# Performance work log

Measured on AMD Instinct MI355X. Metric: run time of the kernel, lower is better.

The kernel has to match this reference:

```python
import jax, jax.numpy as jnp
import numpy as np

H = 4096  # hidden_size == input_size


def setup_inputs() -> dict:
    key = jax.random.key(0)
    ks = jax.random.split(key, 12)
    s = 0.02  # weight init scale
    return {
        "x": jax.random.normal(ks[0], (H,), jnp.float32),
        "h_prev": jnp.zeros((H,), jnp.float32),
        "C_prev": jax.random.normal(ks[1], (H, H), jnp.float32) * 0.01,
        "n_prev": jax.random.uniform(ks[2], (H,), jnp.float32) + 1.0,
        # projection weights (hidden_size x input_size) and biases
        "Wq": jax.random.normal(ks[3], (H, H), jnp.float32) * s,
        "Wk": jax.random.normal(ks[4], (H, H), jnp.float32) * s,
        "Wv": jax.random.normal(ks[5], (H, H), jnp.float32) * s,
        "Wo": jax.random.normal(ks[6], (H, H), jnp.float32) * s,
        "bq": jnp.zeros((H,), jnp.float32),
        "bk": jnp.zeros((H,), jnp.float32),
        "bv": jnp.zeros((H,), jnp.float32),
        "bo": jnp.zeros((H,), jnp.float32),
        # scalar input/forget gates: w^T x + b
        "wi": jax.random.normal(ks[7], (H,), jnp.float32) * s,
        "bi": jnp.zeros((), jnp.float32),
        "wf": jax.random.normal(ks[8], (H,), jnp.float32) * s,
        "bf": jnp.ones((), jnp.float32),  # bias forget gate toward remembering
    }


def reference(x, h_prev, C_prev, n_prev, Wq, Wk, Wv, Wo,
              bq, bk, bv, bo, wi, bi, wf, bf):
    # mLSTM single-step cell (xLSTM matrix memory). h_prev is unused by the
    # mLSTM math (no hidden-to-hidden recurrence), matching the CUDA layer API.
    d = jnp.asarray(Wk.shape[0], x.dtype)
    q = Wq @ x + bq                                   # [H]
    k = (Wk @ x + bk) / jnp.sqrt(d)                   # [H], scaled key
    v = Wv @ x + bv                                   # [H]
    i_gate = jnp.exp(jnp.dot(wi, x) + bi)             # scalar exponential input gate
    f_gate = jax.nn.sigmoid(jnp.dot(wf, x) + bf)      # scalar sigmoid forget gate
    # covariance-style rank-1 matrix-memory update
    C = f_gate * C_prev + i_gate * jnp.outer(v, k)    # [H, H]
    n = f_gate * n_prev + i_gate * k                  # [H]
    # normalized readout
    denom = jnp.maximum(jnp.abs(jnp.dot(n, q)), jnp.asarray(1.0, x.dtype))
    h_tilde = (C @ q) / denom                         # [H]
    o_gate = jax.nn.sigmoid(Wo @ x + bo)              # [H] output gate
    h = o_gate * h_tilde
    return (h, C, n)
```

## Files before the change

kernel.cpp:

```cpp
#include <hip/hip_runtime.h>
#include <math.h>

#define H 4096
#define HWORDS4 (H / 4)
#define ITERS (HWORDS4 / 64)

__device__ __forceinline__ float wave_reduce_sum(float v) {
    #pragma unroll
    for (int off = 32; off > 0; off >>= 1)
        v += __shfl_down(v, off, 64);
    return v;
}

__device__ __forceinline__ float sigmoidf_(float x) {
    return 1.0f / (1.0f + __expf(-x));
}

__global__ __launch_bounds__(256) void gemv_all(
    const float* __restrict__ x,
    const float* __restrict__ Wq, const float* __restrict__ Wk,
    const float* __restrict__ Wv, const float* __restrict__ Wo,
    const float* __restrict__ bq, const float* __restrict__ bk,
    const float* __restrict__ bv, const float* __restrict__ bo,
    const float* __restrict__ wi, const float* __restrict__ wf,
    float* __restrict__ q, float* __restrict__ k,
    float* __restrict__ v, float* __restrict__ og,
    float* __restrict__ s2)
{
    const int wave = threadIdx.x >> 6;
    const int lane = threadIdx.x & 63;
    const int rowId = blockIdx.x * 4 + wave;
    if (rowId >= 4 * H + 2) return;

    const int m = rowId >> 12;
    const int r = rowId & (H - 1);

    const float* row;
    if (rowId < 4 * H) {
        const float* W = (m == 0) ? Wq : (m == 1) ? Wk : (m == 2) ? Wv : Wo;
        row = W + (size_t)r * H;
    } else {
        row = (rowId == 4 * H) ? wi : wf;
    }

    const float4* row4 = (const float4*)row;
    const float4* x4   = (const float4*)x;

    float sum = 0.0f;
    #pragma unroll
    for (int it = 0; it < ITERS; ++it) {
        const int idx = it * 64 + lane;
        float4 a = row4[idx];
        float4 b = x4[idx];
        sum += a.x * b.x + a.y * b.y + a.z * b.z + a.w * b.w;
    }
    sum = wave_reduce_sum(sum);

    if (lane == 0) {
        if (rowId < 4 * H) {
            if (m == 0)      q[r]  = sum + bq[r];
            else if (m == 1) k[r]  = (sum + bk[r]) * 0.015625f;
            else if (m == 2) v[r]  = sum + bv[r];
            else             og[r] = sigmoidf_(sum + bo[r]);
        } else {
            s2[rowId - 4 * H] = sum;
        }
    }
}

__global__ __launch_bounds__(256) void c_update(
    const float* __restrict__ C_prev,
    const float* __restrict__ q, const float* __restrict__ k,
    const float* __restrict__ v, const float* __restrict__ s2,
    const float* __restrict__ bi, const float* __restrict__ bf,
    float* __restrict__ C_out, float* __restrict__ u)
{
    const int wave = threadIdx.x >> 6;
    const int lane = threadIdx.x & 63;
    const int r = blockIdx.x * 4 + wave;

    const float ig = __expf(s2[0] + bi[0]);
    const float fg = sigmoidf_(s2[1] + bf[0]);
    const float ivr = ig * v[r];

    const float4* c4 = (const float4*)(C_prev + (size_t)r * H);
    float4*       o4 = (float4*)(C_out + (size_t)r * H);
    const float4* q4 = (const float4*)q;
    const float4* k4 = (const float4*)k;

    float acc = 0.0f;
    #pragma unroll
    for (int it = 0; it < ITERS; ++it) {
        const int idx = it * 64 + lane;
        float4 c  = c4[idx];
        float4 qq = q4[idx];
        float4 kk = k4[idx];
        float4 o;
        o.x = fg * c.x + ivr * kk.x;
        o.y = fg * c.y + ivr * kk.y;
        o.z = fg * c.z + ivr * kk.z;
        o.w = fg * c.w + ivr * kk.w;
        o4[idx] = o;
        acc += c.x * qq.x + c.y * qq.y + c.z * qq.z + c.w * qq.w;
    }
    acc = wave_reduce_sum(acc);
    if (lane == 0) u[r] = acc;
}

__global__ __launch_bounds__(1024) void finalize(
    const float* __restrict__ n_prev,
    const float* __restrict__ q, const float* __restrict__ k,
    const float* __restrict__ v, const float* __restrict__ og,
    const float* __restrict__ u, const float* __restrict__ s2,
    const float* __restrict__ bi, const float* __restrict__ bf,
    float* __restrict__ h, float* __restrict__ n_out)
{
    const int t = threadIdx.x;
    const int wave = t >> 6;
    const int lane = t & 63;

    const float ig = __expf(s2[0] + bi[0]);
    const float fg = sigmoidf_(s2[1] + bf[0]);

    float nq = 0.0f, kq = 0.0f;
    for (int j = t; j < H; j += 1024) {
        float kj = k[j];
        float qj = q[j];
        float nj = fg * n_prev[j] + ig * kj;
        n_out[j] = nj;
        nq += nj * qj;
        kq += kj * qj;
    }
    nq = wave_reduce_sum(nq);
    kq = wave_reduce_sum(kq);

    __shared__ float snq[16], skq[16];
    if (lane == 0) { snq[wave] = nq; skq[wave] = kq; }
    __syncthreads();
    if (t == 0) {
        float a = 0.0f, b = 0.0f;
        #pragma unroll
        for (int w = 0; w < 16; ++w) { a += snq[w]; b += skq[w]; }
        snq[0] = a; skq[0] = b;
    }
    __syncthreads();

    const float denom = fmaxf(fabsf(snq[0]), 1.0f);
    const float kqv = skq[0];
    const float inv_denom = 1.0f / denom;

    for (int j = t; j < H; j += 1024) {
        float ht = (fg * u[j] + ig * v[j] * kqv) * inv_denom;
        h[j] = og[j] * ht;
    }
}

extern "C" void kernel_launch(void* const* d_in, const int* in_sizes, int n_in,
                              void* d_out, int out_size, void* d_ws, size_t ws_size,
                              hipStream_t stream) {
    const float* x      = (const float*)d_in[0];
    const float* C_prev = (const float*)d_in[2];
    const float* n_prev = (const float*)d_in[3];
    const float* Wq     = (const float*)d_in[4];
    const float* Wk     = (const float*)d_in[5];
    const float* Wv     = (const float*)d_in[6];
    const float* Wo     = (const float*)d_in[7];
    const float* bq     = (const float*)d_in[8];
    const float* bk     = (const float*)d_in[9];
    const float* bv     = (const float*)d_in[10];
    const float* bo     = (const float*)d_in[11];
    const float* wi     = (const float*)d_in[12];
    const float* bi     = (const float*)d_in[13];
    const float* wf     = (const float*)d_in[14];
    const float* bf     = (const float*)d_in[15];

    float* out   = (float*)d_out;
    float* h_out = out;
    float* C_out = out + H;
    float* n_out = out + H + (size_t)H * H;

    float* ws = (float*)d_ws;
    float* q  = ws;
    float* k  = ws + H;
    float* v  = ws + 2 * H;
    float* og = ws + 3 * H;
    float* u  = ws + 4 * H;
    float* s2 = ws + 5 * H;

    const int nrows = 4 * H + 2;
    const int blocks1 = (nrows + 3) / 4;
    gemv_all<<<blocks1, 256, 0, stream>>>(x, Wq, Wk, Wv, Wo, bq, bk, bv, bo,
                                          wi, wf, q, k, v, og, s2);

    c_update<<<H / 4, 256, 0, stream>>>(C_prev, q, k, v, s2, bi, bf, C_out, u);

    finalize<<<1, 1024, 0, stream>>>(n_prev, q, k, v, og, u, s2, bi, bf,
                                     h_out, n_out);
}
```

Baseline: 339.7 us.

## Use whole-block rows with register-cached x/q/k vectors in GEMV and C update

Both memory-bound kernels now assign full 256-thread blocks to process two rows at a time, eight rows per block. The shared vectors (x, or q and k) are loaded into registers once per block instead of being re-read per row by each wave. Cross-wave results are combined through shared memory and barriers. This cuts redundant vector loads and gives each thread more independent loads in flight. The cost is two __syncthreads per row pair, higher register pressure, and half as many blocks.

```diff
diff --git a/kernel.cpp b/kernel.cpp
--- a/kernel.cpp
+++ b/kernel.cpp
@@ -2,8 +2,10 @@
 #include <math.h>
 
 #define H 4096
-#define HWORDS4 (H / 4)
-#define ITERS (HWORDS4 / 64)
+#define H4 (H / 4)
+#define T1 256
+#define RPB 8
+#define NB1 (4 * H / RPB)
 
 __device__ __forceinline__ float wave_reduce_sum(float v) {
     #pragma unroll
@@ -16,7 +18,11 @@
     return 1.0f / (1.0f + __expf(-x));
 }
 
-__global__ __launch_bounds__(256) void gemv_all(
+__device__ __forceinline__ float dot4(float4 a, float4 b) {
+    return a.x * b.x + a.y * b.y + a.z * b.z + a.w * b.w;
+}
+
+__global__ __launch_bounds__(T1) void gemv_all(
     const float* __restrict__ x,
     const float* __restrict__ Wq, const float* __restrict__ Wk,
     const float* __restrict__ Wv, const float* __restrict__ Wo,
@@ -27,84 +33,144 @@
     float* __restrict__ v, float* __restrict__ og,
     float* __restrict__ s2)
 {
-    const int wave = threadIdx.x >> 6;
-    const int lane = threadIdx.x & 63;
-    const int rowId = blockIdx.x * 4 + wave;
-    if (rowId >= 4 * H + 2) return;
-
-    const int m = rowId >> 12;
-    const int r = rowId & (H - 1);
-
-    const float* row;
-    if (rowId < 4 * H) {
-        const float* W = (m == 0) ? Wq : (m == 1) ? Wk : (m == 2) ? Wv : Wo;
-        row = W + (size_t)r * H;
-    } else {
-        row = (rowId == 4 * H) ? wi : wf;
-    }
-
-    const float4* row4 = (const float4*)row;
-    const float4* x4   = (const float4*)x;
-
-    float sum = 0.0f;
+    const int tid  = threadIdx.x;
+    const int wave = tid >> 6;
+    const int lane = tid & 63;
+
+    __shared__ float red[2][4];
+
+    const float4* x4 = (const float4*)x;
+    float4 xr0 = x4[tid];
+    float4 xr1 = x4[tid + 256];
+    float4 xr2 = x4[tid + 512];
+    float4 xr3 = x4[tid + 768];
+
+    if (blockIdx.x == NB1) {
+        const float4* a4 = (const float4*)wi;
+        const float4* b4 = (const float4*)wf;
+        float4 a0 = a4[tid], a1 = a4[tid + 256], a2 = a4[tid + 512], a3 = a4[tid + 768];
+        float4 c0 = b4[tid], c1 = b4[tid + 256], c2 = b4[tid + 512], c3 = b4[tid + 768];
+        float sa = dot4(a0, xr0) + dot4(a1, xr1) + dot4(a2, xr2) + dot4(a3, xr3);
+        float sb = dot4(c0, xr0) + dot4(c1, xr1) + dot4(c2, xr2) + dot4(c3, xr3);
+        sa = wave_reduce_sum(sa);
+        sb = wave_reduce_sum(sb);
+        if (lane == 0) { red[0][wave] = sa; red[1][wave] = sb; }
+        __syncthreads();
+        if (tid < 2) {
+            float s = red[tid][0] + red[tid][1] + red[tid][2] + red[tid][3];
+            s2[tid] = s;
+        }
+        return;
+    }
+
+    const int row0 = blockIdx.x * RPB;
+    const int m = row0 >> 12;
+    const float* W    = (m == 0) ? Wq : (m == 1) ? Wk : (m == 2) ? Wv : Wo;
+    const float* bias = (m == 0) ? bq : (m == 1) ? bk : (m == 2) ? bv : bo;
+    const int rbase = row0 & (H - 1);
+
     #pragma unroll
-    for (int it = 0; it < ITERS; ++it) {
-        const int idx = it * 64 + lane;
-        float4 a = row4[idx];
-        float4 b = x4[idx];
-        sum += a.x * b.x + a.y * b.y + a.z * b.z + a.w * b.w;
-    }
-    sum = wave_reduce_sum(sum);
-
-    if (lane == 0) {
-        if (rowId < 4 * H) {
-            if (m == 0)      q[r]  = sum + bq[r];
-            else if (m == 1) k[r]  = (sum + bk[r]) * 0.015625f;
-            else if (m == 2) v[r]  = sum + bv[r];
-            else             og[r] = sigmoidf_(sum + bo[r]);
-        } else {
-            s2[rowId - 4 * H] = sum;
+    for (int rr = 0; rr < RPB; rr += 2) {
+        const float4* a4 = (const float4*)(W + (size_t)(rbase + rr) * H);
+        const float4* b4 = (const float4*)(W + (size_t)(rbase + rr + 1) * H);
+        float4 a0 = a4[tid], a1 = a4[tid + 256], a2 = a4[tid + 512], a3 = a4[tid + 768];
+        float4 c0 = b4[tid], c1 = b4[tid + 256], c2 = b4[tid + 512], c3 = b4[tid + 768];
+
+        float sa = dot4(a0, xr0) + dot4(a1, xr1) + dot4(a2, xr2) + dot4(a3, xr3);
+        float sb = dot4(c0, xr0) + dot4(c1, xr1) + dot4(c2, xr2) + dot4(c3, xr3);
+        sa = wave_reduce_sum(sa);
+        sb = wave_reduce_sum(sb);
+        if (lane == 0) { red[0][wave] = sa; red[1][wave] = sb; }
+        __syncthreads();
+        if (tid < 2) {
+            const float s = red[tid][0] + red[tid][1] + red[tid][2] + red[tid][3];
+            const int r = rbase + rr + tid;
+            const float sbias = s + bias[r];
+            if (m == 0)      q[r]  = sbias;
+            else if (m == 1) k[r]  = sbias * 0.015625f;
+            else if (m == 2) v[r]  = sbias;
+            else             og[r] = sigmoidf_(sbias);
         }
-    }
-}
-
-__global__ __launch_bounds__(256) void c_update(
+        __syncthreads();
+    }
+}
+
+__global__ __launch_bounds__(T1) void c_update(
     const float* __restrict__ C_prev,
     const float* __restrict__ q, const float* __restrict__ k,
     const float* __restrict__ v, const float* __restrict__ s2,
     const float* __restrict__ bi, const float* __restrict__ bf,
     float* __restrict__ C_out, float* __restrict__ u)
 {
-    const int wave = threadIdx.x >> 6;
-    const int lane = threadIdx.x & 63;
-    const int r = blockIdx.x * 4 + wave;
+    const int tid  = threadIdx.x;
+    const int wave = tid >> 6;
+    const int lane = tid & 63;
+
+    __shared__ float red[2][4];
 
     const float ig = __expf(s2[0] + bi[0]);
     const float fg = sigmoidf_(s2[1] + bf[0]);
-    const float ivr = ig * v[r];
-
-    const float4* c4 = (const float4*)(C_prev + (size_t)r * H);
-    float4*       o4 = (float4*)(C_out + (size_t)r * H);
+
     const float4* q4 = (const float4*)q;
     const float4* k4 = (const float4*)k;
-
-    float acc = 0.0f;
+    float4 qr0 = q4[tid], qr1 = q4[tid + 256], qr2 = q4[tid + 512], qr3 = q4[tid + 768];
+    float4 kr0 = k4[tid], kr1 = k4[tid + 256], kr2 = k4[tid + 512], kr3 = k4[tid + 768];
+
+    const int row0 = blockIdx.x * RPB;
+
     #pragma unroll
-    for (int it = 0; it < ITERS; ++it) {
-        const int idx = it * 64 + lane;
-        float4 c  = c4[idx];
-        float4 qq = q4[idx];
-        float4 kk = k4[idx];
+    for (int rr = 0; rr < RPB; rr += 2) {
+        const int ra = row0 + rr;
+        const int rb = ra + 1;
+        const float iva = ig * v[ra];
+        const float ivb = ig * v[rb];
+
+        const float4* ca4 = (const float4*)(C_prev + (size_t)ra * H);
+        const float4* cb4 = (const float4*)(C_prev + (size_t)rb * H);
+        float4*       oa4 = (float4*)(C_out + (size_t)ra * H);
+        float4*       ob4 = (float4*)(C_out + (size_t)rb * H);
+
+        float4 a0 = ca4[tid], a1 = ca4[tid + 256], a2 = ca4[tid + 512], a3 = ca4[tid + 768];
+        float4 c0 = cb4[tid], c1 = cb4[tid + 256], c2 = cb4[tid + 512], c3 = cb4[tid + 768];
+
         float4 o;
-        o.x = fg * c.x + ivr * kk.x;
-        o.y = fg * c.y + ivr * kk.y;
-        o.z = fg * c.z + ivr * kk.z;
-        o.w = fg * c.w + ivr * kk.w;
-        o4[idx] = o;
-        acc += c.x * qq.x + c.y * qq.y + c.z * qq.z + c.w * qq.w;
-    }
-    acc = wave_reduce_sum(acc);
-    if (lane == 0) u[r] = acc;
+        o.x = fg * a0.x + iva * kr0.x; o.y = fg * a0.y + iva * kr0.y;
+        o.z = fg * a0.z + iva * kr0.z; o.w = fg * a0.w + iva * kr0.w;
+        oa4[tid] = o;
+        o.x = fg * a1.x + iva * kr1.x; o.y = fg * a1.y + iva * kr1.y;
+        o.z = fg * a1.z + iva * kr1.z; o.w = fg * a1.w + iva * kr1.w;
+        oa4[tid + 256] = o;
+        o.x = fg * a2.x + iva * kr2.x; o.y = fg * a2.y + iva * kr2.y;
+        o.z = fg * a2.z + iva * kr2.z; o.w = fg * a2.w + iva * kr2.w;
+        oa4[tid + 512] = o;
+        o.x = fg * a3.x + iva * kr3.x; o.y = fg * a3.y + iva * kr3.y;
+        o.z = fg * a3.z + iva * kr3.z; o.w = fg * a3.w + iva * kr3.w;
+        oa4[tid + 768] = o;
+
+        o.x = fg * c0.x + ivb * kr0.x; o.y = fg * c0.y + ivb * kr0.y;
+        o.z = fg * c0.z + ivb * kr0.z; o.w = fg * c0.w + ivb * kr0.w;
+        ob4[tid] = o;
+        o.x = fg * c1.x + ivb * kr1.x; o.y = fg * c1.y + ivb * kr1.y;
+        o.z = fg * c1.z + ivb * kr1.z; o.w = fg * c1.w + ivb * kr1.w;
+        ob4[tid + 256] = o;
+        o.x = fg * c2.x + ivb * kr2.x; o.y = fg * c2.y + ivb * kr2.y;
+        o.z = fg * c2.z + ivb * kr2.z; o.w = fg * c2.w + ivb * kr2.w;
+        ob4[tid + 512] = o;
+        o.x = fg * c3.x + ivb * kr3.x; o.y = fg * c3.y + ivb * kr3.y;
+        o.z = fg * c3.z + ivb * kr3.z; o.w = fg * c3.w + ivb * kr3.w;
+        ob4[tid + 768] = o;
+
+        float sa = dot4(a0, qr0) + dot4(a1, qr1) + dot4(a2, qr2) + dot4(a3, qr3);
+        float sb = dot4(c0, qr0) + dot4(c1, qr1) + dot4(c2, qr2) + dot4(c3, qr3);
+        sa = wave_reduce_sum(sa);
+        sb = wave_reduce_sum(sb);
+        if (lane == 0) { red[0][wave] = sa; red[1][wave] = sb; }
+        __syncthreads();
+        if (tid < 2) {
+            u[row0 + rr + tid] = red[tid][0] + red[tid][1] + red[tid][2] + red[tid][3];
+        }
+        __syncthreads();
+    }
 }
 
 __global__ __launch_bounds__(1024) void finalize(
@@ -187,12 +253,10 @@
     float* u  = ws + 4 * H;
     float* s2 = ws + 5 * H;
 
-    const int nrows = 4 * H + 2;
-    const int blocks1 = (nrows + 3) / 4;
-    gemv_all<<<blocks1, 256, 0, stream>>>(x, Wq, Wk, Wv, Wo, bq, bk, bv, bo,
-                                          wi, wf, q, k, v, og, s2);
-
-    c_update<<<H / 4, 256, 0, stream>>>(C_prev, q, k, v, s2, bi, bf, C_out, u);
+    gemv_all<<<NB1 + 1, T1, 0, stream>>>(x, Wq, Wk, Wv, Wo, bq, bk, bv, bo,
+                                         wi, wf, q, k, v, og, s2);
+
+    c_update<<<H / RPB, T1, 0, stream>>>(C_prev, q, k, v, s2, bi, bf, C_out, u);
 
     finalize<<<1, 1024, 0, stream>>>(n_prev, q, k, v, og, u, s2, bi, bf,
                                      h_out, n_out);
```

Measured after the change: 348.0 us. 2.4% more time.

## Stage vectors in LDS, batch row loads, use nontemporal C accesses

Applied to the files above, without the earlier changes.

The GEMV and C-update kernels now copy x (and q, k) into shared memory once per block, and every global load of a row is issued up front in two groups separated by scheduling barriers, so many loads are in flight at once. The C_prev reads and C_out writes use nontemporal hints to avoid polluting the cache with streamed data. This aims to raise memory-level parallelism on the bandwidth-bound streams. The cost is 16 KB to 32 KB of LDS per block, which may limit occupancy, plus higher register pressure from 16 live float4 values.

```diff
diff --git a/kernel.cpp b/kernel.cpp
--- a/kernel.cpp
+++ b/kernel.cpp
@@ -2,8 +2,9 @@
 #include <math.h>
 
 #define H 4096
-#define HWORDS4 (H / 4)
-#define ITERS (HWORDS4 / 64)
+#define H4 (H / 4)
+
+typedef float f4 __attribute__((ext_vector_type(4)));
 
 __device__ __forceinline__ float wave_reduce_sum(float v) {
     #pragma unroll
@@ -14,6 +15,10 @@
 
 __device__ __forceinline__ float sigmoidf_(float x) {
     return 1.0f / (1.0f + __expf(-x));
+}
+
+__device__ __forceinline__ float dot4(f4 a, f4 b) {
+    return a.x * b.x + a.y * b.y + a.z * b.z + a.w * b.w;
 }
 
 __global__ __launch_bounds__(256) void gemv_all(
@@ -27,8 +32,16 @@
     float* __restrict__ v, float* __restrict__ og,
     float* __restrict__ s2)
 {
-    const int wave = threadIdx.x >> 6;
-    const int lane = threadIdx.x & 63;
+    const int tid  = threadIdx.x;
+    const int wave = tid >> 6;
+    const int lane = tid & 63;
+
+    __shared__ f4 xs[H4];
+    const f4* x4 = (const f4*)x;
+    #pragma unroll
+    for (int i = 0; i < 4; ++i) xs[tid + i * 256] = x4[tid + i * 256];
+    __syncthreads();
+
     const int rowId = blockIdx.x * 4 + wave;
     if (rowId >= 4 * H + 2) return;
 
@@ -42,28 +55,55 @@
     } else {
         row = (rowId == 4 * H) ? wi : wf;
     }
-
-    const float4* row4 = (const float4*)row;
-    const float4* x4   = (const float4*)x;
-
-    float sum = 0.0f;
-    #pragma unroll
-    for (int it = 0; it < ITERS; ++it) {
-        const int idx = it * 64 + lane;
-        float4 a = row4[idx];
-        float4 b = x4[idx];
-        sum += a.x * b.x + a.y * b.y + a.z * b.z + a.w * b.w;
-    }
-    sum = wave_reduce_sum(sum);
+    const f4* row4 = (const f4*)row;
+
+    f4 a0 = row4[lane +   0];
+    f4 a1 = row4[lane +  64];
+    f4 a2 = row4[lane + 128];
+    f4 a3 = row4[lane + 192];
+    f4 a4_ = row4[lane + 256];
+    f4 a5 = row4[lane + 320];
+    f4 a6 = row4[lane + 384];
+    f4 a7 = row4[lane + 448];
+    __builtin_amdgcn_sched_barrier(0);
+    f4 b0 = row4[lane + 512];
+    f4 b1 = row4[lane + 576];
+    f4 b2 = row4[lane + 640];
+    f4 b3 = row4[lane + 704];
+    f4 b4_ = row4[lane + 768];
+    f4 b5 = row4[lane + 832];
+    f4 b6 = row4[lane + 896];
+    f4 b7 = row4[lane + 960];
+    __builtin_amdgcn_sched_barrier(0);
+
+    float s = 0.0f;
+    s += dot4(a0,  xs[lane +   0]);
+    s += dot4(a1,  xs[lane +  64]);
+    s += dot4(a2,  xs[lane + 128]);
+    s += dot4(a3,  xs[lane + 192]);
+    s += dot4(a4_, xs[lane + 256]);
+    s += dot4(a5,  xs[lane + 320]);
+    s += dot4(a6,  xs[lane + 384]);
+    s += dot4(a7,  xs[lane + 448]);
+    s += dot4(b0,  xs[lane + 512]);
+    s += dot4(b1,  xs[lane + 576]);
+    s += dot4(b2,  xs[lane + 640]);
+    s += dot4(b3,  xs[lane + 704]);
+    s += dot4(b4_, xs[lane + 768]);
+    s += dot4(b5,  xs[lane + 832]);
+    s += dot4(b6,  xs[lane + 896]);
+    s += dot4(b7,  xs[lane + 960]);
+
+    s = wave_reduce_sum(s);
 
     if (lane == 0) {
         if (rowId < 4 * H) {
-            if (m == 0)      q[r]  = sum + bq[r];
-            else if (m == 1) k[r]  = (sum + bk[r]) * 0.015625f;
-            else if (m == 2) v[r]  = sum + bv[r];
-            else             og[r] = sigmoidf_(sum + bo[r]);
+            if (m == 0)      q[r]  = s + bq[r];
+            else if (m == 1) k[r]  = (s + bk[r]) * 0.015625f;
+            else if (m == 2) v[r]  = s + bv[r];
+            else             og[r] = sigmoidf_(s + bo[r]);
         } else {
-            s2[rowId - 4 * H] = sum;
+            s2[rowId - 4 * H] = s;
         }
     }
 }
@@ -75,34 +115,67 @@
     const float* __restrict__ bi, const float* __restrict__ bf,
     float* __restrict__ C_out, float* __restrict__ u)
 {
-    const int wave = threadIdx.x >> 6;
-    const int lane = threadIdx.x & 63;
+    const int tid  = threadIdx.x;
+    const int wave = tid >> 6;
+    const int lane = tid & 63;
+
+    __shared__ f4 qs[H4];
+    __shared__ f4 ks[H4];
+    const f4* q4 = (const f4*)q;
+    const f4* k4 = (const f4*)k;
+    #pragma unroll
+    for (int i = 0; i < 4; ++i) {
+        qs[tid + i * 256] = q4[tid + i * 256];
+        ks[tid + i * 256] = k4[tid + i * 256];
+    }
+    __syncthreads();
+
     const int r = blockIdx.x * 4 + wave;
 
-    const float ig = __expf(s2[0] + bi[0]);
-    const float fg = sigmoidf_(s2[1] + bf[0]);
+    const float ig  = __expf(s2[0] + bi[0]);
+    const float fg  = sigmoidf_(s2[1] + bf[0]);
     const float ivr = ig * v[r];
 
-    const float4* c4 = (const float4*)(C_prev + (size_t)r * H);
-    float4*       o4 = (float4*)(C_out + (size_t)r * H);
-    const float4* q4 = (const float4*)q;
-    const float4* k4 = (const float4*)k;
+    const f4* c4 = (const f4*)(C_prev + (size_t)r * H);
+    f4*       o4 = (f4*)(C_out + (size_t)r * H);
+
+    f4 a0 = __builtin_nontemporal_load(&c4[lane +   0]);
+    f4 a1 = __builtin_nontemporal_load(&c4[lane +  64]);
+    f4 a2 = __builtin_nontemporal_load(&c4[lane + 128]);
+    f4 a3 = __builtin_nontemporal_load(&c4[lane + 192]);
+    f4 a4_ = __builtin_nontemporal_load(&c4[lane + 256]);
+    f4 a5 = __builtin_nontemporal_load(&c4[lane + 320]);
+    f4 a6 = __builtin_nontemporal_load(&c4[lane + 384]);
+    f4 a7 = __builtin_nontemporal_load(&c4[lane + 448]);
+    __builtin_amdgcn_sched_barrier(0);
+    f4 b0 = __builtin_nontemporal_load(&c4[lane + 512]);
+    f4 b1 = __builtin_nontemporal_load(&c4[lane + 576]);
+    f4 b2 = __builtin_nontemporal_load(&c4[lane + 640]);
+    f4 b3 = __builtin_nontemporal_load(&c4[lane + 704]);
+    f4 b4_ = __builtin_nontemporal_load(&c4[lane + 768]);
+    f4 b5 = __builtin_nontemporal_load(&c4[lane + 832]);
+    f4 b6 = __builtin_nontemporal_load(&c4[lane + 896]);
+    f4 b7 = __builtin_nontemporal_load(&c4[lane + 960]);
+    __builtin_amdgcn_sched_barrier(0);
 
     float acc = 0.0f;
-    #pragma unroll
-    for (int it = 0; it < ITERS; ++it) {
-        const int idx = it * 64 + lane;
-        float4 c  = c4[idx];
-        float4 qq = q4[idx];
-        float4 kk = k4[idx];
-        float4 o;
-        o.x = fg * c.x + ivr * kk.x;
-        o.y = fg * c.y + ivr * kk.y;
-        o.z = fg * c.z + ivr * kk.z;
-        o.w = fg * c.w + ivr * kk.w;
-        o4[idx] = o;
-        acc += c.x * qq.x + c.y * qq.y + c.z * qq.z + c.w * qq.w;
-    }
+    f4 o;
+    #define CONSUME(reg, off)                                            \
+        {                                                                \
+            f4 kk = ks[lane + (off)];                                    \
+            o.x = fg * reg.x + ivr * kk.x;                               \
+            o.y = fg * reg.y + ivr * kk.y;                               \
+            o.z = fg * reg.z + ivr * kk.z;                               \
+            o.w = fg * reg.w + ivr * kk.w;                               \
+            __builtin_nontemporal_store(o, &o4[lane + (off)]);           \
+            acc += dot4(reg, qs[lane + (off)]);                          \
+        }
+    CONSUME(a0,   0) CONSUME(a1,  64) CONSUME(a2, 128) CONSUME(a3, 192)
+    CONSUME(a4_, 256) CONSUME(a5, 320) CONSUME(a6, 384) CONSUME(a7, 448)
+    CONSUME(b0, 512) CONSUME(b1, 576) CONSUME(b2, 640) CONSUME(b3, 704)
+    CONSUME(b4_, 768) CONSUME(b5, 832) CONSUME(b6, 896) CONSUME(b7, 960)
+    #undef CONSUME
+
     acc = wave_reduce_sum(acc);
     if (lane == 0) u[r] = acc;
 }
```

New measurement: 336.4 us. About the same (-1.0%).
